# Optimization experiments

Measured on AMD Instinct MI355X. Metric: run time of the kernel, lower is better.

Reference implementation:

```python
import jax, jax.numpy as jnp
import numpy as np

EPS = 1e-5  # torch InstanceNorm2d default eps

def instance_norm(x):
    # per-sample, per-channel normalization over spatial dims (affine=False)
    m = jnp.mean(x, axis=(2, 3), keepdims=True)
    v = jnp.var(x, axis=(2, 3), keepdims=True)
    return (x - m) * jax.lax.rsqrt(v + EPS)

def conv2d(x, w, b, stride, pad):
    y = jax.lax.conv_general_dilated(
        x, w, (stride, stride), [(pad, pad), (pad, pad)],
        dimension_numbers=('NCHW', 'OIHW', 'NCHW'))
    return y + b[None, :, None, None]

def res_block(x, w1, b1, w2, b2):
    out = conv2d(jax.nn.relu(instance_norm(x)), w1, b1, 1, 1)
    out = conv2d(jax.nn.relu(instance_norm(out)), w2, b2, 1, 1)
    return out + x

def res_block_strided(x, w1, b1, w2, b2, ws, bs):
    out = conv2d(jax.nn.relu(instance_norm(x)), w1, b1, 2, 1)
    out = conv2d(jax.nn.relu(instance_norm(out)), w2, b2, 1, 1)
    return out + conv2d(x, ws, bs, 2, 0)  # 1x1 strided skip projection

def setup_inputs() -> dict:
    key = jax.random.key(0)
    ks = jax.random.split(key, 12)
    B, N, C, H, W = 64, 1, 3, 256, 256
    TEXT, EMB, F, HEADS = 256, 512, 32, 5
    FH, FW = H // 16, W // 16  # 16, 16
    def rn(k, shape, scale=0.05):
        return jax.random.normal(k, shape, dtype=jnp.float32) * scale
    z = lambda *s: jnp.zeros(s, jnp.float32)
    return {
        'x': jax.random.normal(ks[0], (B, N, C, H, W), jnp.float32),
        'text_vector': jax.random.normal(ks[1], (B, TEXT), jnp.float32),
        'conv1_w': rn(ks[2], (F, C, 7, 7)),
        'conv1_b': z(F),
        'rbs_w1': rn(ks[3], (3, F, F, 3, 3)),  # 3 strided resblocks
        'rbs_b1': z(3, F),
        'rbs_w2': rn(ks[4], (3, F, F, 3, 3)),
        'rbs_b2': z(3, F),
        'rbs_ws': rn(ks[5], (3, F, F, 1, 1)),
        'rbs_bs': z(3, F),
        'rb_w1': rn(ks[6], (2, F, F, 3, 3)),  # 2 plain resblocks
        'rb_b1': z(2, F),
        'rb_w2': rn(ks[7], (2, F, F, 3, 3)),
        'rb_b2': z(2, F),
        'attn_w': rn(ks[8], (HEADS, FH * FW, TEXT)),  # torch Linear [out,in] per head
        'attn_b': z(HEADS, FH * FW),
        'final_w': rn(ks[9], (EMB, FH * FW * HEADS)),
        'final_b': z(EMB),
    }

def reference(x, text_vector, conv1_w, conv1_b, rbs_w1, rbs_b1, rbs_w2, rbs_b2,
              rbs_ws, rbs_bs, rb_w1, rb_b1, rb_w2, rb_b2, attn_w, attn_b,
              final_w, final_b):
    B, N, C, H, W = x.shape
    feat = x.reshape(B, N * C, H, W)
    feat = instance_norm(feat)
    feat = conv2d(feat, conv1_w, conv1_b, 2, 3)
    # block1 = strided + plain; block2 = strided + plain; block3 = strided
    feat = res_block_strided(feat, rbs_w1[0], rbs_b1[0], rbs_w2[0], rbs_b2[0], rbs_ws[0], rbs_bs[0])
    feat = res_block(feat, rb_w1[0], rb_b1[0], rb_w2[0], rb_b2[0])
    feat = res_block_strided(feat, rbs_w1[1], rbs_b1[1], rbs_w2[1], rbs_b2[1], rbs_ws[1], rbs_bs[1])
    feat = res_block(feat, rb_w1[1], rb_b1[1], rb_w2[1], rb_b2[1])
    feat = res_block_strided(feat, rbs_w1[2], rbs_b1[2], rbs_w2[2], rbs_b2[2], rbs_ws[2], rbs_bs[2])
    # feat: [B, 32, FH, FW]
    HEADS = attn_w.shape[0]
    FH, FW = feat.shape[2], feat.shape[3]
    # sigmoid-gated spatial attention logits per head: [B, HEADS, FH, FW]
    a = jax.nn.sigmoid(jnp.einsum('bt,hot->bho', text_vector, attn_w) + attn_b[None])
    a = a.reshape(B, HEADS, FH, FW)
    # channel scores: spatial sum of gate * feature -> [B, HEADS, C]
    scores = jnp.einsum('bhij,bcij->bhc', a, feat)
    probs = jax.nn.softmax(scores, axis=-1)  # old F.softmax over channel dim
    # weighted channel sum -> per-head attention map [B, HEADS, FH, FW]
    amaps = jnp.einsum('bhc,bcij->bhij', probs, feat)
    out = amaps.reshape(B, -1) @ final_w.T + final_b
    return out
```

## Files before the change

### kernel.cpp

```cpp
#include <hip/hip_runtime.h>
#include <cstdint>
#include <cstddef>

#define INORM_EPS 1e-5f

typedef _Float16 f16;
typedef f16 f16x8 __attribute__((ext_vector_type(8)));
typedef f16 f16x4 __attribute__((ext_vector_type(4)));
typedef float f32x4 __attribute__((ext_vector_type(4)));

__global__ __launch_bounds__(256) void prep_stats(
    const float* __restrict__ rbs_w1, const float* __restrict__ rbs_w2,
    const float* __restrict__ rb_w1, const float* __restrict__ rb_w2,
    const float* __restrict__ rbs_ws, const float* __restrict__ conv1_w,
    const float* __restrict__ x, float2* __restrict__ SP,
    f16* __restrict__ wp3, f16* __restrict__ wp1, f16* __restrict__ wp7,
    float2* __restrict__ SPx8) {
  const int bx = blockIdx.x;
  if (bx >= 480) {
    const int g = bx - 480;
    const int map = g >> 3, chunk = g & 7;
    const float4* p = (const float4*)(x + (size_t)map * 65536 + (size_t)chunk * 8192);
    float s = 0.f, ss = 0.f;
    for (int i = threadIdx.x; i < 2048; i += 256) {
      float4 v = p[i];
      s += v.x + v.y + v.z + v.w;
      ss += v.x * v.x + v.y * v.y + v.z * v.z + v.w * v.w;
    }
    __shared__ float r0[256], r1[256];
    r0[threadIdx.x] = s;
    r1[threadIdx.x] = ss;
    __syncthreads();
    for (int off = 128; off > 0; off >>= 1) {
      if ((int)threadIdx.x < off) {
        r0[threadIdx.x] += r0[threadIdx.x + off];
        r1[threadIdx.x] += r1[threadIdx.x + off];
      }
      __syncthreads();
    }
    if (threadIdx.x == 0) SPx8[map * 8 + chunk] = make_float2(r0[0], r1[0]);
    return;
  }
  int i = bx * 256 + threadIdx.x;
  if (i < 20480) { SP[i] = make_float2(0.f, 0.f); return; }
  i -= 20480;
  if (i < 92160) {
    int mat = i / 9216, r = i % 9216;
    int p = r >> 10, f = (r >> 9) & 1, l = (r >> 3) & 63, j = r & 7;
    int co = f * 16 + (l & 15), ci = (l >> 4) * 8 + j;
    const float* src; int m;
    if (mat < 3) { src = rbs_w1; m = mat; }
    else if (mat < 6) { src = rbs_w2; m = mat - 3; }
    else if (mat < 8) { src = rb_w1; m = mat - 6; }
    else { src = rb_w2; m = mat - 8; }
    wp3[i] = (f16)src[m * 9216 + co * 288 + ci * 9 + p];
    return;
  }
  i -= 92160;
  if (i < 3072) {
    int mat = i / 1024, r = i % 1024;
    int f = r >> 9, l = (r >> 3) & 63, j = r & 7;
    wp1[i] = (f16)rbs_ws[mat * 1024 + (f * 16 + (l & 15)) * 32 + (l >> 4) * 8 + j];
    return;
  }
  i -= 3072;
  if (i >= 7168) return;
  int ky = i >> 10, f = (i >> 9) & 1, l = (i >> 3) & 63, j = i & 7;
  int k = (l >> 4) * 8 + j, kx = k >> 2, ci = k & 3;
  float v = 0.f;
  if (kx < 7 && ci < 3) v = conv1_w[(f * 16 + (l & 15)) * 147 + ci * 49 + ky * 7 + kx];
  wp7[i] = (f16)v;
}

template <int W, int SKIP, int RPB>
__global__ __launch_bounds__(256) void conv3r(
    const f16* __restrict__ Rin, const float2* __restrict__ SPin, float inv_hw,
    const f16* __restrict__ wp, const float* __restrict__ bias,
    const float* __restrict__ bias2, const f16* __restrict__ skip,
    const f16* __restrict__ wps, f16* __restrict__ Rout,
    float2* __restrict__ ostats) {
  constexpr int TPR = W / 16;
  constexpr int LEN = (RPB * TPR) / 4;
  const int t = threadIdx.x, w = t >> 6, l = t & 63;
  const int n = l & 15, q = l >> 4;
  const int b = blockIdx.z;
  const int tx = w % TPR;
  const int y0 = blockIdx.x * RPB + (w / TPR) * LEN;
  const int x = (tx << 4) + n;
  const f16* Rb = Rin + (size_t)b * W * W * 32;

  f16x8 sc, sh;
#pragma unroll
  for (int j = 0; j < 8; j++) {
    float2 s = SPin[b * 32 + q * 8 + j];
    float mean = s.x * inv_hw;
    float rstd = rsqrtf(s.y * inv_hw - mean * mean + INORM_EPS);
    sc[j] = (f16)rstd;
    sh[j] = (f16)(-mean * rstd);
  }

  f16x8 wf[18];
#pragma unroll
  for (int i = 0; i < 18; i++) wf[i] = *(const f16x8*)(wp + i * 512 + l * 8);
  f16x8 wsf0, wsf1;
  if (SKIP == 2) {
    wsf0 = *(const f16x8*)(wps + l * 8);
    wsf1 = *(const f16x8*)(wps + 512 + l * 8);
  }
  float b0 = bias[n], b1 = bias[16 + n];
  if (SKIP == 2) { b0 += bias2[n]; b1 += bias2[16 + n]; }

  f16* ro = Rout + (size_t)b * W * W * 32;
  const f16* sb = skip ? skip + (size_t)b * (SKIP == 2 ? 4 : 1) * W * W * 32 : nullptr;

  bool okc[3];
#pragma unroll
  for (int kx = 0; kx < 3; kx++) okc[kx] = (unsigned)(x + kx - 1) < (unsigned)W;

  auto rowload = [&](int gy, f16x8* dst) {
    int gyc = min(max(gy, 0), W - 1);
#pragma unroll
    for (int kx = 0; kx < 3; kx++) {
      int gxc = min(max(x + kx - 1, 0), W - 1);
      dst[kx] = *(const f16x8*)(Rb + ((size_t)gyc * W + gxc) * 32 + q * 8);
    }
  };
  auto rownorm = [&](int gy, const f16x8* src, f16x8* dst) {
    bool okr = (unsigned)gy < (unsigned)W;
#pragma unroll
    for (int kx = 0; kx < 3; kx++) {
      f16x8 v = src[kx] * sc + sh;
#pragma unroll
      for (int e = 0; e < 8; e++) v[e] = v[e] > (f16)0 ? v[e] : (f16)0;
      f16x8 z = {};
      dst[kx] = (okr && okc[kx]) ? v : z;
    }
  };

  float sm0 = 0.f, sq0 = 0.f, sm1 = 0.f, sq1 = 0.f;
  f16x8 win[9];
  f16x8 pf[2][3];
#pragma unroll
  for (int jj = 0; jj < 3; jj++) rowload(y0 + jj - 1, &win[jj * 3]);
  if (LEN > 1) rowload(y0 + 2, pf[0]);
#pragma unroll
  for (int jj = 0; jj < 3; jj++) rownorm(y0 + jj - 1, &win[jj * 3], &win[jj * 3]);

#pragma unroll
  for (int i = 0; i < LEN; i++) {
    int y = y0 + i;
    if (i + 2 < LEN) rowload(y0 + i + 3, pf[(i + 1) & 1]);
    f32x4 acc0 = {0.f, 0.f, 0.f, 0.f}, acc1 = {0.f, 0.f, 0.f, 0.f};
#pragma unroll
    for (int ky = 0; ky < 3; ky++) {
      int slot = (i + ky) % 3;
#pragma unroll
      for (int kx = 0; kx < 3; kx++) {
        f16x8 a = win[slot * 3 + kx];
        acc0 = __builtin_amdgcn_mfma_f32_16x16x32_f16(a, wf[2 * (ky * 3 + kx)], acc0, 0, 0, 0);
        acc1 = __builtin_amdgcn_mfma_f32_16x16x32_f16(a, wf[2 * (ky * 3 + kx) + 1], acc1, 0, 0, 0);
      }
    }
    if (SKIP == 2) {
      const int Ws = 2 * W;
      f16x8 as = *(const f16x8*)(sb + ((size_t)(2 * y) * Ws + 2 * x) * 32 + q * 8);
      acc0 = __builtin_amdgcn_mfma_f32_16x16x32_f16(as, wsf0, acc0, 0, 0, 0);
      acc1 = __builtin_amdgcn_mfma_f32_16x16x32_f16(as, wsf1, acc1, 0, 0, 0);
    }
#pragma unroll
    for (int r = 0; r < 4; r++) {
      size_t px = (size_t)y * W + (tx << 4) + q * 4 + r;
      float v0 = acc0[r] + b0;
      float v1 = acc1[r] + b1;
      if (SKIP == 1) {
        v0 += (float)sb[px * 32 + n];
        v1 += (float)sb[px * 32 + 16 + n];
      }
      ro[px * 32 + n] = (f16)v0;
      ro[px * 32 + 16 + n] = (f16)v1;
      sm0 += v0; sq0 += v0 * v0;
      sm1 += v1; sq1 += v1 * v1;
    }
    if (i + 1 < LEN) rownorm(y0 + i + 2, pf[i & 1], &win[(i % 3) * 3]);
  }
  if (ostats) {
    sm0 += __shfl_xor(sm0, 16); sm0 += __shfl_xor(sm0, 32);
    sq0 += __shfl_xor(sq0, 16); sq0 += __shfl_xor(sq0, 32);
    sm1 += __shfl_xor(sm1, 16); sm1 += __shfl_xor(sm1, 32);
    sq1 += __shfl_xor(sq1, 16); sq1 += __shfl_xor(sq1, 32);
    if (l < 16) {
      atomicAdd(&ostats[b * 32 + n].x, sm0);
      atomicAdd(&ostats[b * 32 + n].y, sq0);
      atomicAdd(&ostats[b * 32 + 16 + n].x, sm1);
      atomicAdd(&ostats[b * 32 + 16 + n].y, sq1);
    }
  }
}

template <int WIN, int STRIDE, int SKIP, int RPB>
__global__ __launch_bounds__(256) void conv3n(
    const f16* __restrict__ Rin, const float2* __restrict__ SPin, float inv_hw,
    const f16* __restrict__ wp, const float* __restrict__ bias,
    const float* __restrict__ bias2, const f16* __restrict__ skip,
    const f16* __restrict__ wps, f16* __restrict__ Rout,
    float2* __restrict__ ostats) {
  constexpr int WOUT = WIN / STRIDE;
  constexpr int TPR = WOUT / 16;
  constexpr int UNITS = TPR * RPB;
  constexpr int U = UNITS / 4;
  static_assert(U >= 1, "need at least one unit per wave");
  constexpr int NB = (U >= 3) ? 3 : ((U >= 2) ? 2 : 1);
  const int t = threadIdx.x, w = t >> 6, l = t & 63;
  const int n = l & 15, q = l >> 4;
  const int b = blockIdx.z;
  const int yb = blockIdx.x * RPB;
  const f16* Rb = Rin + (size_t)b * WIN * WIN * 32;

  f16x8 sc, sh;
#pragma unroll
  for (int j = 0; j < 8; j++) {
    float2 s = SPin[b * 32 + q * 8 + j];
    float mean = s.x * inv_hw;
    float rstd = rsqrtf(s.y * inv_hw - mean * mean + INORM_EPS);
    sc[j] = (f16)rstd;
    sh[j] = (f16)(-mean * rstd);
  }

  f16x8 wf[18];
#pragma unroll
  for (int i = 0; i < 18; i++) wf[i] = *(const f16x8*)(wp + i * 512 + l * 8);
  f16x8 wsf0, wsf1;
  if (SKIP == 2) {
    wsf0 = *(const f16x8*)(wps + l * 8);
    wsf1 = *(const f16x8*)(wps + 512 + l * 8);
  }
  float b0 = bias[n], b1 = bias[16 + n];
  if (SKIP == 2) { b0 += bias2[n]; b1 += bias2[16 + n]; }

  f16* ro = Rout + (size_t)b * WOUT * WOUT * 32;
  const f16* sb = skip ? skip + (size_t)b * (SKIP == 2 ? 4 : 1) * WOUT * WOUT * 32 : nullptr;

  auto load_u = [&](int u, f16x8* a) {
    int ty = u / TPR, tx = u % TPR;
    int y = yb + ty;
#pragma unroll
    for (int kx = 0; kx < 3; kx++) {
      int gx = STRIDE * ((tx << 4) + n) + kx - 1;
      int gxc = min(max(gx, 0), WIN - 1);
#pragma unroll
      for (int ky = 0; ky < 3; ky++) {
        int gy = STRIDE * y + ky - 1;
        int gyc = min(max(gy, 0), WIN - 1);
        a[ky * 3 + kx] = *(const f16x8*)(Rb + ((size_t)gyc * WIN + gxc) * 32 + q * 8);
      }
    }
  };
  auto norm_u = [&](int u, f16x8* a) {
    int ty = u / TPR, tx = u % TPR;
    int y = yb + ty;
#pragma unroll
    for (int kx = 0; kx < 3; kx++) {
      int gx = STRIDE * ((tx << 4) + n) + kx - 1;
      bool okx = (unsigned)gx < (unsigned)WIN;
#pragma unroll
      for (int ky = 0; ky < 3; ky++) {
        int gy = STRIDE * y + ky - 1;
        bool ok = okx && ((unsigned)gy < (unsigned)WIN);
        f16x8 v = a[ky * 3 + kx] * sc + sh;
#pragma unroll
        for (int e = 0; e < 8; e++) v[e] = v[e] > (f16)0 ? v[e] : (f16)0;
        f16x8 z = {};
        a[ky * 3 + kx] = ok ? v : z;
      }
    }
  };

  float sm0 = 0.f, sq0 = 0.f, sm1 = 0.f, sq1 = 0.f;
  f16x8 buf[NB][9];
  load_u(w, buf[0]);
  if (U > 1) load_u(w + 4, buf[1 % NB]);
#pragma unroll
  for (int i = 0; i < U; i++) {
    int u = w + 4 * i;
    if (i + 2 < U) load_u(u + 8, buf[(i + 2) % NB]);
    f16x8* a = buf[i % NB];
    norm_u(u, a);
    int ty = u / TPR, tx = u % TPR;
    int y = yb + ty, x0 = tx << 4;
    f32x4 acc0 = {0.f, 0.f, 0.f, 0.f}, acc1 = {0.f, 0.f, 0.f, 0.f};
#pragma unroll
    for (int p = 0; p < 9; p++) {
      acc0 = __builtin_amdgcn_mfma_f32_16x16x32_f16(a[p], wf[2 * p], acc0, 0, 0, 0);
      acc1 = __builtin_amdgcn_mfma_f32_16x16x32_f16(a[p], wf[2 * p + 1], acc1, 0, 0, 0);
    }
    if (SKIP == 2) {
      const int Ws = 2 * WOUT;
      f16x8 as = *(const f16x8*)(sb + ((size_t)(2 * y) * Ws + 2 * (x0 + n)) * 32 + q * 8);
      acc0 = __builtin_amdgcn_mfma_f32_16x16x32_f16(as, wsf0, acc0, 0, 0, 0);
      acc1 = __builtin_amdgcn_mfma_f32_16x16x32_f16(as, wsf1, acc1, 0, 0, 0);
    }
#pragma unroll
    for (int r = 0; r < 4; r++) {
      size_t px = (size_t)y * WOUT + x0 + q * 4 + r;
      float v0 = acc0[r] + b0;
      float v1 = acc1[r] + b1;
      if (SKIP == 1) {
        v0 += (float)sb[px * 32 + n];
        v1 += (float)sb[px * 32 + 16 + n];
      }
      ro[px * 32 + n] = (f16)v0;
      ro[px * 32 + 16 + n] = (f16)v1;
      sm0 += v0; sq0 += v0 * v0;
      sm1 += v1; sq1 += v1 * v1;
    }
  }
  if (ostats) {
    sm0 += __shfl_xor(sm0, 16); sm0 += __shfl_xor(sm0, 32);
    sq0 += __shfl_xor(sq0, 16); sq0 += __shfl_xor(sq0, 32);
    sm1 += __shfl_xor(sm1, 16); sm1 += __shfl_xor(sm1, 32);
    sq1 += __shfl_xor(sq1, 16); sq1 += __shfl_xor(sq1, 32);
    if (l < 16) {
      atomicAdd(&ostats[b * 32 + n].x, sm0);
      atomicAdd(&ostats[b * 32 + n].y, sq0);
      atomicAdd(&ostats[b * 32 + 16 + n].x, sm1);
      atomicAdd(&ostats[b * 32 + 16 + n].y, sq1);
    }
  }
}

__global__ __launch_bounds__(256) void conv7(
    const float* __restrict__ x, const float2* __restrict__ SPx8,
    const f16* __restrict__ wp, const float* __restrict__ bias,
    f16* __restrict__ Rout, float2* __restrict__ ostats) {
  __shared__ f16 lds[13 * 131 * 8];
  const int t = threadIdx.x, w = t >> 6, l = t & 63;
  const int n = l & 15, q = l >> 4;
  const int b = blockIdx.z;
  const int yb = blockIdx.x * 4;
  const float* Xb = x + (size_t)b * 3 * 65536;
  float mn[3], rs[3];
#pragma unroll
  for (int ci = 0; ci < 3; ci++) {
    float sx = 0.f, sxx = 0.f;
#pragma unroll
    for (int c = 0; c < 8; c++) {
      float2 v = SPx8[(b * 3 + ci) * 8 + c];
      sx += v.x; sxx += v.y;
    }
    mn[ci] = sx * (1.f / 65536.f);
    rs[ci] = rsqrtf(sxx * (1.f / 65536.f) - mn[ci] * mn[ci] + INORM_EPS);
  }
  f16x8 wf[14];
#pragma unroll
  for (int i = 0; i < 14; i++) wf[i] = *(const f16x8*)(wp + i * 512 + l * 8);
  float b0 = bias[n], b1 = bias[16 + n];

  for (int idx = t; idx < 13 * 262; idx += 256) {
    int ri = idx / 262, cl = idx - ri * 262;
    int row = 2 * yb - 3 + ri, col = cl - 3;
    bool ok = ((unsigned)row < 256u) && ((unsigned)col < 256u);
    f16x4 v = {};
    if (ok) {
      const float* p = Xb + (size_t)row * 256 + col;
      v[0] = (f16)((p[0] - mn[0]) * rs[0]);
      v[1] = (f16)((p[65536] - mn[1]) * rs[1]);
      v[2] = (f16)((p[131072] - mn[2]) * rs[2]);
    }
    *(f16x4*)(lds + ((ri * 131 + (cl >> 1)) * 8) + (cl & 1) * 4) = v;
  }
  __syncthreads();

  float sm0 = 0.f, sq0 = 0.f, sm1 = 0.f, sq1 = 0.f;
  f16* ro = Rout + (size_t)b * 16384 * 32;

#pragma unroll
  for (int seg = 0; seg < 2; seg++) {
    const int tx = w + seg * 4;
    const int x0 = tx * 16;
    const int u = x0 + n + q;
#pragma unroll
    for (int i = 0; i < 4; i++) {
      int y = yb + i;
      f32x4 acc0 = {0.f, 0.f, 0.f, 0.f}, acc1 = {0.f, 0.f, 0.f, 0.f};
#pragma unroll
      for (int ky = 0; ky < 7; ky++) {
        f16x8 a = *(const f16x8*)(lds + ((2 * i + ky) * 131 + u) * 8);
        acc0 = __builtin_amdgcn_mfma_f32_16x16x32_f16(a, wf[2 * ky], acc0, 0, 0, 0);
        acc1 = __builtin_amdgcn_mfma_f32_16x16x32_f16(a, wf[2 * ky + 1], acc1, 0, 0, 0);
      }
#pragma unroll
      for (int r = 0; r < 4; r++) {
        size_t px = (size_t)y * 128 + x0 + q * 4 + r;
        float v0 = acc0[r] + b0;
        float v1 = acc1[r] + b1;
        ro[px * 32 + n] = (f16)v0;
        ro[px * 32 + 16 + n] = (f16)v1;
        sm0 += v0; sq0 += v0 * v0;
        sm1 += v1; sq1 += v1 * v1;
      }
    }
  }
  sm0 += __shfl_xor(sm0, 16); sm0 += __shfl_xor(sm0, 32);
  sq0 += __shfl_xor(sq0, 16); sq0 += __shfl_xor(sq0, 32);
  sm1 += __shfl_xor(sm1, 16); sm1 += __shfl_xor(sm1, 32);
  sq1 += __shfl_xor(sq1, 16); sq1 += __shfl_xor(sq1, 32);
  if (l < 16) {
    atomicAdd(&ostats[b * 32 + n].x, sm0);
    atomicAdd(&ostats[b * 32 + n].y, sq0);
    atomicAdd(&ostats[b * 32 + 16 + n].x, sm1);
    atomicAdd(&ostats[b * 32 + 16 + n].y, sq1);
  }
}

__global__ __launch_bounds__(256) void gates_kernel(
    const float* __restrict__ text, const float* __restrict__ attn_w,
    const float* __restrict__ attn_b, float* __restrict__ G) {
  __shared__ float s_text[64 * 257];
  __shared__ float s_w[16 * 256];
  const int t = threadIdx.x, wv = t >> 6, lane = t & 63;
  const int o0 = blockIdx.x * 16;
  for (int d = t; d < 16384; d += 256) {
    int b = d >> 8, k = d & 255;
    s_text[b * 257 + k] = text[d];
  }
  for (int d = t; d < 4096; d += 256) s_w[d] = attn_w[(size_t)o0 * 256 + d];
  __syncthreads();
  float acc[4];
#pragma unroll
  for (int j = 0; j < 4; j++) acc[j] = attn_b[o0 + wv * 4 + j];
  for (int k = 0; k < 256; k++) {
    float tv = s_text[lane * 257 + k];
#pragma unroll
    for (int j = 0; j < 4; j++) acc[j] = fmaf(s_w[(wv * 4 + j) * 256 + k], tv, acc[j]);
  }
#pragma unroll
  for (int j = 0; j < 4; j++) {
    int o = o0 + wv * 4 + j;
    G[o * 64 + lane] = 1.f / (1.f + __expf(-acc[j]));
  }
}

__global__ __launch_bounds__(256) void scores_kernel(
    const f16* __restrict__ feat, const float* __restrict__ G,
    float* __restrict__ amapT) {
  __shared__ float s_feat[256 * 33];
  __shared__ float s_gate[1280];
  __shared__ float s_scores[5 * 32];
  __shared__ float s_probs[5 * 32];
  const int b = blockIdx.x;
  const int t = threadIdx.x;

  for (int i = t; i < 8192; i += 256)
    s_feat[(i >> 5) * 33 + (i & 31)] = (float)feat[(size_t)b * 8192 + i];
  for (int i = t; i < 1280; i += 256) s_gate[i] = G[i * 64 + b];
  __syncthreads();

  if (t < 160) {
    int h = t >> 5, c = t & 31;
    float acc = 0.f;
    for (int ij = 0; ij < 256; ij++) acc += s_gate[h * 256 + ij] * s_feat[ij * 33 + c];
    s_scores[t] = acc;
  }
  __syncthreads();

  if (t < 5) {
    float mx = -1e30f;
    for (int c = 0; c < 32; c++) mx = fmaxf(mx, s_scores[t * 32 + c]);
    float sum = 0.f;
    for (int c = 0; c < 32; c++) {
      float e = __expf(s_scores[t * 32 + c] - mx);
      s_probs[t * 32 + c] = e;
      sum += e;
    }
    float inv = 1.f / sum;
    for (int c = 0; c < 32; c++) s_probs[t * 32 + c] *= inv;
  }
  __syncthreads();

  for (int h = 0; h < 5; h++) {
    float acc = 0.f;
    for (int c = 0; c < 32; c++) acc += s_probs[h * 32 + c] * s_feat[t * 33 + c];
    amapT[(h * 256 + t) * 64 + b] = acc;
  }
}

__global__ __launch_bounds__(256) void final_kernel(
    const float* __restrict__ amapT, const float* __restrict__ final_w,
    const float* __restrict__ final_b, float* __restrict__ out) {
  __shared__ float s_w[4 * 1280];
  __shared__ float s_red[4][4][64];
  const int t = threadIdx.x, wv = t >> 6, lane = t & 63;
  const int e0 = blockIdx.x * 4;
  for (int d = t; d < 5120; d += 256) s_w[d] = final_w[(size_t)e0 * 1280 + d];
  __syncthreads();
  const int k0 = wv * 320;
  float acc[4] = {0.f, 0.f, 0.f, 0.f};
  for (int k = k0; k < k0 + 320; k++) {
    float av = amapT[k * 64 + lane];
#pragma unroll
    for (int e = 0; e < 4; e++) acc[e] = fmaf(s_w[e * 1280 + k], av, acc[e]);
  }
#pragma unroll
  for (int e = 0; e < 4; e++) s_red[wv][e][lane] = acc[e];
  __syncthreads();
  if (wv == 0) {
#pragma unroll
    for (int e = 0; e < 4; e++) {
      float v = s_red[0][e][lane] + s_red[1][e][lane] + s_red[2][e][lane] +
                s_red[3][e][lane] + final_b[e0 + e];
      out[(size_t)lane * 512 + e0 + e] = v;
    }
  }
}

extern "C" void kernel_launch(void* const* d_in, const int* in_sizes, int n_in,
                              void* d_out, int out_size, void* d_ws, size_t ws_size,
                              hipStream_t stream) {
  (void)in_sizes; (void)n_in; (void)out_size; (void)ws_size;
  const float* x       = (const float*)d_in[0];
  const float* text    = (const float*)d_in[1];
  const float* conv1_w = (const float*)d_in[2];
  const float* conv1_b = (const float*)d_in[3];
  const float* rbs_w1  = (const float*)d_in[4];
  const float* rbs_b1  = (const float*)d_in[5];
  const float* rbs_w2  = (const float*)d_in[6];
  const float* rbs_b2  = (const float*)d_in[7];
  const float* rbs_ws  = (const float*)d_in[8];
  const float* rbs_bs  = (const float*)d_in[9];
  const float* rb_w1   = (const float*)d_in[10];
  const float* rb_b1   = (const float*)d_in[11];
  const float* rb_w2   = (const float*)d_in[12];
  const float* rb_b2   = (const float*)d_in[13];
  const float* attn_w  = (const float*)d_in[14];
  const float* attn_b  = (const float*)d_in[15];
  const float* final_w = (const float*)d_in[16];
  const float* final_b = (const float*)d_in[17];
  float* out = (float*)d_out;

  char* wsb = (char*)d_ws;
  float2* SPx8 = (float2*)(wsb + 0);
  f16*   R128 = (f16*)(wsb + 35145728);
  f16*   R64a = (f16*)(wsb + 102254592);
  f16*   R64b = (f16*)(wsb + 119031808);
  f16*   R64c = (f16*)(wsb + 135809024);
  f16*   R32a = (f16*)(wsb + 152586240);
  f16*   R32b = (f16*)(wsb + 156780544);
  f16*   R32c = (f16*)(wsb + 160974848);
  f16*   R16a = (f16*)(wsb + 165169152);
  f16*   R16b = (f16*)(wsb + 166217728);
  float2* SP  = (float2*)(wsb + 167266304);
  f16*   wp3  = (f16*)(wsb + 167431680);
  f16*   wp1  = (f16*)(wsb + 167616000);
  f16*   wp7  = (f16*)(wsb + 167622144);
  float* G     = (float*)(wsb + 167636480);
  float* amapT = (float*)(wsb + 167964160);
  float2* SP0 = SP + 0 * 2048;
  float2* SP1 = SP + 1 * 2048;
  float2* SP2 = SP + 2 * 2048;
  float2* SP3 = SP + 3 * 2048;
  float2* SP4 = SP + 4 * 2048;
  float2* SP5 = SP + 5 * 2048;
  float2* SP6 = SP + 6 * 2048;
  float2* SP7 = SP + 7 * 2048;
  float2* SP8 = SP + 8 * 2048;
  float2* SP9 = SP + 9 * 2048;

  prep_stats<<<2016, 256, 0, stream>>>(rbs_w1, rbs_w2, rb_w1, rb_w2, rbs_ws,
                                       conv1_w, x, SP, wp3, wp1, wp7, SPx8);

  conv7<<<dim3(32, 1, 64), 256, 0, stream>>>(x, SPx8, wp7, conv1_b, R128, SP0);

  conv3n<128, 2, 0, 4><<<dim3(16, 1, 64), 256, 0, stream>>>(
      R128, SP0, 1.f / 16384.f, wp3, rbs_b1, nullptr, nullptr, nullptr, R64a, SP1);
  conv3r<64, 2, 8><<<dim3(8, 1, 64), 256, 0, stream>>>(
      R64a, SP1, 1.f / 4096.f, wp3 + 3 * 9216, rbs_b2, rbs_bs, R128, wp1, R64b, SP2);

  conv3r<64, 0, 8><<<dim3(8, 1, 64), 256, 0, stream>>>(
      R64b, SP2, 1.f / 4096.f, wp3 + 6 * 9216, rb_b1, nullptr, nullptr, nullptr, R64c, SP3);
  conv3r<64, 1, 8><<<dim3(8, 1, 64), 256, 0, stream>>>(
      R64c, SP3, 1.f / 4096.f, wp3 + 8 * 9216, rb_b2, nullptr, R64b, nullptr, R64a, SP4);

  conv3n<64, 2, 0, 4><<<dim3(8, 1, 64), 256, 0, stream>>>(
      R64a, SP4, 1.f / 4096.f, wp3 + 1 * 9216, rbs_b1 + 32, nullptr, nullptr, nullptr, R32a, SP5);
  conv3r<32, 2, 8><<<dim3(4, 1, 64), 256, 0, stream>>>(
      R32a, SP5, 1.f / 1024.f, wp3 + 4 * 9216, rbs_b2 + 32, rbs_bs + 32, R64a, wp1 + 1024, R32b, SP6);

  conv3r<32, 0, 8><<<dim3(4, 1, 64), 256, 0, stream>>>(
      R32b, SP6, 1.f / 1024.f, wp3 + 7 * 9216, rb_b1 + 32, nullptr, nullptr, nullptr, R32c, SP7);
  conv3r<32, 1, 8><<<dim3(4, 1, 64), 256, 0, stream>>>(
      R32c, SP7, 1.f / 1024.f, wp3 + 9 * 9216, rb_b2 + 32, nullptr, R32b, nullptr, R32a, SP8);

  conv3n<32, 2, 0, 8><<<dim3(2, 1, 64), 256, 0, stream>>>(
      R32a, SP8, 1.f / 1024.f, wp3 + 2 * 9216, rbs_b1 + 64, nullptr, nullptr, nullptr, R16a, SP9);
  conv3n<16, 1, 2, 8><<<dim3(2, 1, 64), 256, 0, stream>>>(
      R16a, SP9, 1.f / 256.f, wp3 + 5 * 9216, rbs_b2 + 64, rbs_bs + 64, R32a, wp1 + 2048, R16b, nullptr);

  gates_kernel<<<80, 256, 0, stream>>>(text, attn_w, attn_b, G);
  scores_kernel<<<64, 256, 0, stream>>>(R16b, G, amapT);
  final_kernel<<<128, 256, 0, stream>>>(amapT, final_w, final_b, out);
}
```

Measured before the change: 320.8 us.

## Double output rows per conv7 block and prefetch second input slab during compute

The 7x7 stem conv now computes 8 output rows per block instead of 4, halving the grid and reusing the overlapping 13-row halo. The extra 8 input rows are loaded from global memory into registers before the first half is computed, then normalized and written to LDS before the second half runs. This overlaps global load latency with MFMA work and cuts redundant halo loads, at the cost of more LDS, more live registers, and fewer blocks in flight.

Result: faster. 313.2 us (-2.4%).

```diff
diff --git a/kernel.cpp b/kernel.cpp
--- a/kernel.cpp
+++ b/kernel.cpp
@@ -332,11 +332,11 @@
     const float* __restrict__ x, const float2* __restrict__ SPx8,
     const f16* __restrict__ wp, const float* __restrict__ bias,
     f16* __restrict__ Rout, float2* __restrict__ ostats) {
-  __shared__ f16 lds[13 * 131 * 8];
+  __shared__ f16 lds[21 * 131 * 8];
   const int t = threadIdx.x, w = t >> 6, l = t & 63;
   const int n = l & 15, q = l >> 4;
   const int b = blockIdx.z;
-  const int yb = blockIdx.x * 4;
+  const int yb = blockIdx.x * 8;
   const float* Xb = x + (size_t)b * 3 * 65536;
   float mn[3], rs[3];
 #pragma unroll
@@ -370,36 +370,75 @@
   }
   __syncthreads();
 
+  float ub0[9], ub1[9], ub2[9];
+#pragma unroll
+  for (int it = 0; it < 9; it++) {
+    int idx = t + it * 256;
+    int ri = idx / 262, cl = idx - ri * 262;
+    int row = 2 * yb + 10 + ri, col = cl - 3;
+    bool ok = (idx < 2096) && (row < 256) && ((unsigned)col < 256u);
+    const float* p = Xb + (size_t)(ok ? row : 0) * 256 + (ok ? col : 0);
+    ub0[it] = p[0];
+    ub1[it] = p[65536];
+    ub2[it] = p[131072];
+  }
+
   float sm0 = 0.f, sq0 = 0.f, sm1 = 0.f, sq1 = 0.f;
   f16* ro = Rout + (size_t)b * 16384 * 32;
 
-#pragma unroll
-  for (int seg = 0; seg < 2; seg++) {
-    const int tx = w + seg * 4;
-    const int x0 = tx * 16;
-    const int u = x0 + n + q;
-#pragma unroll
-    for (int i = 0; i < 4; i++) {
-      int y = yb + i;
-      f32x4 acc0 = {0.f, 0.f, 0.f, 0.f}, acc1 = {0.f, 0.f, 0.f, 0.f};
-#pragma unroll
-      for (int ky = 0; ky < 7; ky++) {
-        f16x8 a = *(const f16x8*)(lds + ((2 * i + ky) * 131 + u) * 8);
-        acc0 = __builtin_amdgcn_mfma_f32_16x16x32_f16(a, wf[2 * ky], acc0, 0, 0, 0);
-        acc1 = __builtin_amdgcn_mfma_f32_16x16x32_f16(a, wf[2 * ky + 1], acc1, 0, 0, 0);
-      }
-#pragma unroll
-      for (int r = 0; r < 4; r++) {
-        size_t px = (size_t)y * 128 + x0 + q * 4 + r;
-        float v0 = acc0[r] + b0;
-        float v1 = acc1[r] + b1;
-        ro[px * 32 + n] = (f16)v0;
-        ro[px * 32 + 16 + n] = (f16)v1;
-        sm0 += v0; sq0 += v0 * v0;
-        sm1 += v1; sq1 += v1 * v1;
-      }
-    }
-  }
+  auto compute4 = [&](int i0) {
+#pragma unroll
+    for (int seg = 0; seg < 2; seg++) {
+      const int tx = w + seg * 4;
+      const int x0 = tx * 16;
+      const int u = x0 + n + q;
+#pragma unroll
+      for (int ii = 0; ii < 4; ii++) {
+        int i = i0 + ii;
+        int y = yb + i;
+        f32x4 acc0 = {0.f, 0.f, 0.f, 0.f}, acc1 = {0.f, 0.f, 0.f, 0.f};
+#pragma unroll
+        for (int ky = 0; ky < 7; ky++) {
+          f16x8 a = *(const f16x8*)(lds + ((2 * i + ky) * 131 + u) * 8);
+          acc0 = __builtin_amdgcn_mfma_f32_16x16x32_f16(a, wf[2 * ky], acc0, 0, 0, 0);
+          acc1 = __builtin_amdgcn_mfma_f32_16x16x32_f16(a, wf[2 * ky + 1], acc1, 0, 0, 0);
+        }
+#pragma unroll
+        for (int r = 0; r < 4; r++) {
+          size_t px = (size_t)y * 128 + x0 + q * 4 + r;
+          float v0 = acc0[r] + b0;
+          float v1 = acc1[r] + b1;
+          ro[px * 32 + n] = (f16)v0;
+          ro[px * 32 + 16 + n] = (f16)v1;
+          sm0 += v0; sq0 += v0 * v0;
+          sm1 += v1; sq1 += v1 * v1;
+        }
+      }
+    }
+  };
+
+  compute4(0);
+
+#pragma unroll
+  for (int it = 0; it < 9; it++) {
+    int idx = t + it * 256;
+    if (idx < 2096) {
+      int ri = idx / 262, cl = idx - ri * 262;
+      int row = 2 * yb + 10 + ri, col = cl - 3;
+      bool ok = (row < 256) && ((unsigned)col < 256u);
+      f16x4 v = {};
+      if (ok) {
+        v[0] = (f16)((ub0[it] - mn[0]) * rs[0]);
+        v[1] = (f16)((ub1[it] - mn[1]) * rs[1]);
+        v[2] = (f16)((ub2[it] - mn[2]) * rs[2]);
+      }
+      *(f16x4*)(lds + (((13 + ri) * 131 + (cl >> 1)) * 8) + (cl & 1) * 4) = v;
+    }
+  }
+  __syncthreads();
+
+  compute4(4);
+
   sm0 += __shfl_xor(sm0, 16); sm0 += __shfl_xor(sm0, 32);
   sq0 += __shfl_xor(sq0, 16); sq0 += __shfl_xor(sq0, 32);
   sm1 += __shfl_xor(sm1, 16); sm1 += __shfl_xor(sm1, 32);
@@ -568,7 +607,7 @@
   prep_stats<<<2016, 256, 0, stream>>>(rbs_w1, rbs_w2, rb_w1, rb_w2, rbs_ws,
                                        conv1_w, x, SP, wp3, wp1, wp7, SPx8);
 
-  conv7<<<dim3(32, 1, 64), 256, 0, stream>>>(x, SPx8, wp7, conv1_b, R128, SP0);
+  conv7<<<dim3(16, 1, 64), 256, 0, stream>>>(x, SPx8, wp7, conv1_b, R128, SP0);
 
   conv3n<128, 2, 0, 4><<<dim3(16, 1, 64), 256, 0, stream>>>(
       R128, SP0, 1.f / 16384.f, wp3, rbs_b1, nullptr, nullptr, nullptr, R64a, SP1);
```
